# Kernel optimization log

Hardware: AMD Instinct MI355X
Metric: run time of the kernel (lower is better)

The kernel has to match this reference:

```python
import jax, jax.numpy as jnp
import numpy as np

B, S, D, H = 2, 2048, 1024, 16
HD = D // H  # head_size = 64


def setup_inputs() -> dict:
    key = jax.random.key(0)
    ks = jax.random.split(key, 11)
    s = 1.0 / np.sqrt(D)
    inp = {
        "q": jax.random.normal(ks[0], (B, S, D), jnp.float32),
        "k": jax.random.normal(ks[1], (B, S, D), jnp.float32),
        "v": jax.random.normal(ks[2], (B, S, D), jnp.float32),
        "Wq": jax.random.normal(ks[3], (D, D), jnp.float32) * s,
        "bq": jax.random.normal(ks[4], (D,), jnp.float32) * s,
        "Wk": jax.random.normal(ks[5], (D, D), jnp.float32) * s,
        "bk": jax.random.normal(ks[6], (D,), jnp.float32) * s,
        "Wv": jax.random.normal(ks[7], (D, D), jnp.float32) * s,
        "bv": jax.random.normal(ks[8], (D,), jnp.float32) * s,
        "Wo": jax.random.normal(ks[9], (D, D), jnp.float32) * s,
        "bo": jax.random.normal(ks[10], (D,), jnp.float32) * s,
    }
    return inp


def reference(q, k, v, Wq, bq, Wk, bk, Wv, bv, Wo, bo):
    # project and split heads: [B,S,D] -> [B,H,S,HD]
    def split_heads(x, W, b):
        y = x @ W.T + b
        return y.reshape(B, S, H, HD).transpose(0, 2, 1, 3)

    qh = split_heads(q, Wq, bq)
    kh = split_heads(k, Wk, bk)
    vh = split_heads(v, Wv, bv)

    scale = 1.0 / jnp.sqrt(jnp.asarray(HD, qh.dtype))
    scores = jnp.einsum("bhqd,bhkd->bhqk", qh, kh) * scale  # [B,H,S,S]
    weights = jax.nn.softmax(scores, axis=-1)
    out = jnp.einsum("bhqk,bhkd->bhqd", weights, vh)  # [B,H,S,HD]
    out = out.transpose(0, 2, 1, 3).reshape(B, S, D)
    return out @ Wo.T + bo
```

## Files before the change

### kernel.cpp

```cpp
#include <hip/hip_runtime.h>

typedef __attribute__((ext_vector_type(4))) float f32x4;
typedef __attribute__((ext_vector_type(8))) short bf16x8;
typedef __attribute__((ext_vector_type(8))) unsigned short u16x8;
typedef __attribute__((ext_vector_type(4))) unsigned short u16x4;
typedef __attribute__((ext_vector_type(4))) unsigned int u32x4;
typedef unsigned short ushort_t;

#define LOG2E 1.4426950408889634f

__device__ inline unsigned short f2bf(float x) {
  union { float f; unsigned int u; } v; v.f = x;
  unsigned int r = v.u + 0x7fffu + ((v.u >> 16) & 1u);
  return (unsigned short)(r >> 16);
}

__device__ inline unsigned cvtpk_bf16(float a, float b) {
  unsigned r;
  asm("v_cvt_pk_bf16_f32 %0, %1, %2" : "=v"(r) : "v"(a), "v"(b));
  return r;
}

__device__ inline void gload_lds16(const void* g, void* l) {
  __builtin_amdgcn_global_load_lds(
      (const __attribute__((address_space(1))) unsigned int*)g,
      (__attribute__((address_space(3))) unsigned int*)l, 16, 0, 0);
}

__device__ inline void cvt_body(const float* __restrict__ src, ushort_t* __restrict__ dst, int i) {
  const f32x4* s = (const f32x4*)src;
  f32x4 a = s[2 * i], b = s[2 * i + 1];
  u16x8 o;
#pragma unroll
  for (int j = 0; j < 4; ++j) { o[j] = f2bf(a[j]); o[4 + j] = f2bf(b[j]); }
  *(u16x8*)(dst + (size_t)i * 8) = o;
}

__global__ __launch_bounds__(256) void cvt_bf16(const float* __restrict__ src,
                                                ushort_t* __restrict__ dst, int n8) {
  int i = blockIdx.x * 256 + threadIdx.x;
  if (i < n8) cvt_body(src, dst, i);
}

__global__ __launch_bounds__(256) void cvt_all(const float* __restrict__ q,
                                               const float* __restrict__ k,
                                               const float* __restrict__ v,
                                               const float* __restrict__ Wq,
                                               const float* __restrict__ Wk,
                                               const float* __restrict__ Wv,
                                               const float* __restrict__ Wo,
                                               ushort_t* __restrict__ Xb,
                                               ushort_t* __restrict__ Wb, int nx8) {
  int i = blockIdx.x * 256 + threadIdx.x;
  int z = blockIdx.y;
  if (z < 3) {
    if (i < nx8) cvt_body(z == 0 ? q : (z == 1 ? k : v), Xb + (size_t)z * nx8 * 8, i);
  } else {
    int w = i >> 17, off = i & 131071;
    const float* s = w == 0 ? Wq : (w == 1 ? Wk : (w == 2 ? Wv : Wo));
    cvt_body(s, Wb + (size_t)w * 1048576, off);
  }
}

template <typename F>
__device__ inline void gemm_core64(const ushort_t* __restrict__ A, const ushort_t* __restrict__ W,
                                   int m0, int n0, ushort_t* As, ushort_t* Bs, F&& mfma_step) {
  constexpr int K = 1024;
  const int tid = threadIdx.x, lane = tid & 63, wid = tid >> 6;
  const int r8 = lane >> 3;
  const int p8 = lane & 7;
  const int scol = (p8 ^ r8) * 8;
  for (int k0 = 0; k0 < K; k0 += 64) {
#pragma unroll
    for (int c = 0; c < 4; ++c) {
      int i = wid * 4 + c;
      int row = i * 8 + r8;
      gload_lds16(A + (size_t)(m0 + row) * K + k0 + scol, &As[i * 512]);
      gload_lds16(W + (size_t)(n0 + row) * K + k0 + scol, &Bs[i * 512]);
    }
    __syncthreads();
    mfma_step(As, Bs);
    __syncthreads();
  }
}

__global__ __launch_bounds__(256) void proj_gemm(const ushort_t* __restrict__ Abase, int aStride,
                                                 const ushort_t* __restrict__ Wall, int wStride,
                                                 const float* __restrict__ bq,
                                                 const float* __restrict__ bk,
                                                 const float* __restrict__ bv, float qs,
                                                 ushort_t* __restrict__ outQ,
                                                 ushort_t* __restrict__ outK,
                                                 ushort_t* __restrict__ outV, int zofs) {
  __shared__ __attribute__((aligned(16))) ushort_t As[128 * 64];
  __shared__ __attribute__((aligned(16))) ushort_t Bs[128 * 64];
  const int z = blockIdx.z + zofs;
  const ushort_t* A = Abase + (size_t)z * aStride;
  const ushort_t* W = Wall + (size_t)z * wStride;
  const float* bias = z == 0 ? bq : (z == 1 ? bk : bv);
  const float scale = z == 0 ? qs : 1.0f;
  ushort_t* out = z == 0 ? outQ : (z == 1 ? outK : outV);
  const int mode = z == 2 ? 1 : 0;

  const int tid = threadIdx.x, lane = tid & 63, wid = tid >> 6;
  const int m0 = blockIdx.x * 128, n0 = blockIdx.y * 128;
  const int wm = wid >> 1, wn = wid & 1;
  const int qr = lane & 15, kq = lane >> 4;
  f32x4 acc[4][4] = {};

  gemm_core64(A, W, m0, n0, As, Bs, [&](ushort_t* as, ushort_t* bs) {
#pragma unroll
    for (int h = 0; h < 2; ++h) {
      bf16x8 a[4], b[4];
#pragma unroll
      for (int f = 0; f < 4; ++f) {
        int ra = wm * 64 + f * 16 + qr;
        a[f] = *(const bf16x8*)&as[ra * 64 + (((h * 4 + kq) ^ (ra & 7)) * 8)];
        int rb = wn * 64 + f * 16 + qr;
        b[f] = *(const bf16x8*)&bs[rb * 64 + (((h * 4 + kq) ^ (rb & 7)) * 8)];
      }
#pragma unroll
      for (int i = 0; i < 4; ++i)
#pragma unroll
        for (int j = 0; j < 4; ++j)
          acc[i][j] = __builtin_amdgcn_mfma_f32_16x16x32_bf16(a[i], b[j], acc[i][j], 0, 0, 0);
    }
  });

  const int cm = m0 + wm * 64, cn = n0 + wn * 64;
#pragma unroll
  for (int fn = 0; fn < 4; ++fn) {
    int n = cn + fn * 16 + qr;
    float bvv = bias[n];
    int h = n >> 6, hd = n & 63;
#pragma unroll
    for (int fm = 0; fm < 4; ++fm) {
      int m = cm + fm * 16 + kq * 4;
      if (mode == 0) {
#pragma unroll
        for (int r = 0; r < 4; ++r) {
          int mm = m + r, b = mm >> 11, s = mm & 2047;
          out[((size_t)(b * 16 + h) * 2048 + s) * 64 + hd] = f2bf((acc[fm][fn][r] + bvv) * scale);
        }
      } else {
        int b = m >> 11, s = m & 2047;
        u16x4 pk;
#pragma unroll
        for (int r = 0; r < 4; ++r) pk[r] = f2bf((acc[fm][fn][r] + bvv) * scale);
        *(u16x4*)&out[((size_t)(b * 16 + h) * 64 + hd) * 2048 + s] = pk;
      }
    }
  }
}

__global__ __launch_bounds__(256) void gemm_out(const ushort_t* __restrict__ A,
                                                const ushort_t* __restrict__ W,
                                                const float* __restrict__ bias,
                                                float* __restrict__ out) {
  __shared__ __attribute__((aligned(16))) ushort_t As[128 * 64];
  __shared__ __attribute__((aligned(16))) ushort_t Bs[128 * 64];
  const int tid = threadIdx.x, lane = tid & 63, wid = tid >> 6;
  const int m0 = blockIdx.x * 128, n0 = blockIdx.y * 128;
  const int wm = wid >> 1, wn = wid & 1;
  const int qr = lane & 15, kq = lane >> 4;
  f32x4 acc[4][4] = {};

  gemm_core64(A, W, m0, n0, As, Bs, [&](ushort_t* as, ushort_t* bs) {
#pragma unroll
    for (int h = 0; h < 2; ++h) {
      bf16x8 a[4], b[4];
#pragma unroll
      for (int f = 0; f < 4; ++f) {
        int ra = wm * 64 + f * 16 + qr;
        a[f] = *(const bf16x8*)&as[ra * 64 + (((h * 4 + kq) ^ (ra & 7)) * 8)];
        int rb = wn * 64 + f * 16 + qr;
        b[f] = *(const bf16x8*)&bs[rb * 64 + (((h * 4 + kq) ^ (rb & 7)) * 8)];
      }
#pragma unroll
      for (int i = 0; i < 4; ++i)
#pragma unroll
        for (int j = 0; j < 4; ++j)
          acc[i][j] = __builtin_amdgcn_mfma_f32_16x16x32_bf16(a[i], b[j], acc[i][j], 0, 0, 0);
    }
  });

  const int cm = m0 + wm * 64, cn = n0 + wn * 64;
#pragma unroll
  for (int fn = 0; fn < 4; ++fn) {
    int n = cn + fn * 16 + qr;
    float bvv = bias[n];
#pragma unroll
    for (int fm = 0; fm < 4; ++fm) {
      int m = cm + fm * 16 + kq * 4;
#pragma unroll
      for (int r = 0; r < 4; ++r) out[(size_t)(m + r) * 1024 + n] = acc[fm][fn][r] + bvv;
    }
  }
}

__global__ __launch_bounds__(256) void attn_fwd(const ushort_t* __restrict__ Qh,
                                                const ushort_t* __restrict__ Kh,
                                                const ushort_t* __restrict__ Vt,
                                                ushort_t* __restrict__ ctx) {
  constexpr int S = 2048, HD = 64, NT = S / 64;
  __shared__ __attribute__((aligned(16))) ushort_t Ks[2][64 * 64];
  __shared__ __attribute__((aligned(16))) ushort_t Vs[2][64 * 64];

  const int tid = threadIdx.x, lane = tid & 63, wid = tid >> 6;
  const int bh = blockIdx.y, qt = blockIdx.x;
  const size_t head = (size_t)bh * S * HD;
  const ushort_t* Qp = Qh + head;
  const ushort_t* Kp = Kh + head;
  const ushort_t* Vp = Vt + head;

  const int qr = lane & 15, kq = lane >> 4;
  const int q0 = qt * 64 + wid * 16;

  bf16x8 qf[2];
  qf[0] = *(const bf16x8*)&Qp[(size_t)(q0 + qr) * HD + kq * 8];
  qf[1] = *(const bf16x8*)&Qp[(size_t)(q0 + qr) * HD + 32 + kq * 8];

  f32x4 accO[4] = {};
  float mrun = -3e38f, lrun = 0.f;

  const int srow8 = lane >> 3, sp8 = lane & 7;

  for (int t = 0; t < NT; ++t) {
    const int buf = t & 1;
    {
      int kv0 = t == 0 ? 0 : (t + 1) * 64;
      int dbuf = t == 0 ? 0 : buf ^ 1;
      if (t == 0 || t + 1 < NT) {
#pragma unroll
        for (int c = 0; c < 2; ++c) {
          int i = wid * 2 + c;
          int row = i * 8 + srow8;
          int s = sp8 ^ (row & 7);
          gload_lds16(&Kp[(size_t)(kv0 + row) * HD + s * 8], &Ks[dbuf][i * 512]);
          gload_lds16(&Vp[(size_t)row * S + kv0 + s * 8], &Vs[dbuf][i * 512]);
        }
      }
      if (t == 0) {
        __syncthreads();
        if (NT > 1) {
#pragma unroll
          for (int c = 0; c < 2; ++c) {
            int i = wid * 2 + c;
            int row = i * 8 + srow8;
            int s = sp8 ^ (row & 7);
            gload_lds16(&Kp[(size_t)(64 + row) * HD + s * 8], &Ks[1][i * 512]);
            gload_lds16(&Vp[(size_t)row * S + 64 + s * 8], &Vs[1][i * 512]);
          }
        }
      }
    }

    f32x4 sc[4] = {};
    __builtin_amdgcn_s_setprio(1);
#pragma unroll
    for (int fn = 0; fn < 4; ++fn) {
      int rk = fn * 16 + qr;
#pragma unroll
      for (int kh = 0; kh < 2; ++kh) {
        bf16x8 kf = *(const bf16x8*)&Ks[buf][rk * 64 + (((kh * 4 + kq) ^ (rk & 7)) * 8)];
        sc[fn] = __builtin_amdgcn_mfma_f32_16x16x32_bf16(kf, qf[kh], sc[fn], 0, 0, 0);
      }
    }
    __builtin_amdgcn_s_setprio(0);

    float t0 = fmaxf(fmaxf(fmaxf(sc[0][0], sc[0][1]), sc[0][2]), sc[0][3]);
    float t1 = fmaxf(fmaxf(fmaxf(sc[1][0], sc[1][1]), sc[1][2]), sc[1][3]);
    float t2 = fmaxf(fmaxf(fmaxf(sc[2][0], sc[2][1]), sc[2][2]), sc[2][3]);
    float t3 = fmaxf(fmaxf(fmaxf(sc[3][0], sc[3][1]), sc[3][2]), sc[3][3]);
    float pm = fmaxf(fmaxf(t0, t1), fmaxf(t2, t3));
    pm = fmaxf(pm, __shfl_xor(pm, 16, 64));
    pm = fmaxf(pm, __shfl_xor(pm, 32, 64));

    bool need = pm > mrun + 8.0f;
    if (__any(need)) {
      float mn = need ? pm : mrun;
      float sf = __builtin_amdgcn_exp2f(mrun - mn);
      mrun = mn;
#pragma unroll
      for (int f2 = 0; f2 < 4; ++f2) accO[f2] *= sf;
      lrun *= sf;
    }

    float pv[4][4];
    float sum = 0.f;
#pragma unroll
    for (int fn = 0; fn < 4; ++fn)
#pragma unroll
      for (int r = 0; r < 4; ++r) {
        float p = __builtin_amdgcn_exp2f(sc[fn][r] - mrun);
        pv[fn][r] = p;
        sum += p;
      }
    sum += __shfl_xor(sum, 16, 64);
    sum += __shfl_xor(sum, 32, 64);
    lrun += sum;

    unsigned wv[4][2];
#pragma unroll
    for (int fn = 0; fn < 4; ++fn) {
      wv[fn][0] = cvtpk_bf16(pv[fn][0], pv[fn][1]);
      wv[fn][1] = cvtpk_bf16(pv[fn][2], pv[fn][3]);
    }

    __builtin_amdgcn_s_setprio(1);
#pragma unroll
    for (int ks = 0; ks < 2; ++ks) {
      unsigned a0 = wv[2 * ks][0], b0 = wv[2 * ks + 1][0];
      unsigned a1 = wv[2 * ks][1], b1 = wv[2 * ks + 1][1];
      asm volatile("v_permlane32_swap_b32 %0, %1" : "+v"(a0), "+v"(b0));
      asm volatile("v_permlane16_swap_b32 %0, %1" : "+v"(a0), "+v"(b0));
      asm volatile("v_permlane32_swap_b32 %0, %1" : "+v"(a1), "+v"(b1));
      asm volatile("v_permlane16_swap_b32 %0, %1" : "+v"(a1), "+v"(b1));
      u32x4 praw;
      praw[0] = a0; praw[1] = a1; praw[2] = b0; praw[3] = b1;
      bf16x8 pf = __builtin_bit_cast(bf16x8, praw);
#pragma unroll
      for (int f2 = 0; f2 < 4; ++f2) {
        int rv = f2 * 16 + qr;
        bf16x8 vf = *(const bf16x8*)&Vs[buf][rv * 64 + (((ks * 4 + kq) ^ (rv & 7)) * 8)];
        accO[f2] = __builtin_amdgcn_mfma_f32_16x16x32_bf16(vf, pf, accO[f2], 0, 0, 0);
      }
    }
    __builtin_amdgcn_s_setprio(0);
    __syncthreads();
  }

  float inv = 1.0f / lrun;
  const int b = bh >> 4, h = bh & 15;
#pragma unroll
  for (int f2 = 0; f2 < 4; ++f2) {
    u16x4 pk;
#pragma unroll
    for (int r = 0; r < 4; ++r) pk[r] = f2bf(accO[f2][r] * inv);
    int col = h * 64 + f2 * 16 + kq * 4;
    *(u16x4*)&ctx[((size_t)b * 2048 + q0 + qr) * 1024 + col] = pk;
  }
}

extern "C" void kernel_launch(void* const* d_in, const int* in_sizes, int n_in,
                              void* d_out, int out_size, void* d_ws, size_t ws_size,
                              hipStream_t stream) {
  const float* q = (const float*)d_in[0];
  const float* k = (const float*)d_in[1];
  const float* v = (const float*)d_in[2];
  const float* Wq = (const float*)d_in[3];
  const float* bq = (const float*)d_in[4];
  const float* Wk = (const float*)d_in[5];
  const float* bk = (const float*)d_in[6];
  const float* Wv = (const float*)d_in[7];
  const float* bv = (const float*)d_in[8];
  const float* Wo = (const float*)d_in[9];
  const float* bo = (const float*)d_in[10];

  char* ws = (char*)d_ws;
  const size_t MB = 1024 * 1024;
  const int NXE = 4194304;
  const int NWE = 1048576;
  const float qs = 0.125f * LOG2E;
  dim3 gg(32, 8), ga(32, 32);

  if (ws_size >= 56 * MB) {
    ushort_t* Xb = (ushort_t*)(ws);
    ushort_t* Wb = (ushort_t*)(ws + 24 * MB);
    ushort_t* Qh = (ushort_t*)(ws + 32 * MB);
    ushort_t* Kh = (ushort_t*)(ws + 40 * MB);
    ushort_t* Vt = (ushort_t*)(ws + 48 * MB);
    cvt_all<<<dim3(2048, 4), 256, 0, stream>>>(q, k, v, Wq, Wk, Wv, Wo, Xb, Wb, NXE / 8);
    proj_gemm<<<dim3(32, 8, 3), 256, 0, stream>>>(Xb, NXE, Wb, NWE, bq, bk, bv, qs,
                                                  Qh, Kh, Vt, 0);
    attn_fwd<<<ga, 256, 0, stream>>>(Qh, Kh, Vt, Xb);
    gemm_out<<<gg, 256, 0, stream>>>(Xb, Wb + (size_t)3 * NWE, bo, (float*)d_out);
  } else if (ws_size >= 40 * MB) {
    ushort_t* Xb = (ushort_t*)(ws);
    ushort_t* Wb = (ushort_t*)(ws + 8 * MB);
    ushort_t* Qh = (ushort_t*)(ws + 16 * MB);
    ushort_t* Kh = (ushort_t*)(ws + 24 * MB);
    ushort_t* Vt = (ushort_t*)(ws + 32 * MB);
    const float* xs[3] = {q, k, v};
    for (int z = 0; z < 3; ++z) {
      cvt_bf16<<<2048, 256, 0, stream>>>(xs[z], Xb, NXE / 8);
      if (z == 0)
        cvt_all<<<dim3(2048, 1), 256, 0, stream>>>(q, k, v, Wq, Wk, Wv, Wo, Xb, Wb, 0);
      proj_gemm<<<dim3(32, 8, 1), 256, 0, stream>>>(Xb, 0, Wb, NWE, bq, bk, bv, qs,
                                                    Qh, Kh, Vt, z);
    }
    attn_fwd<<<ga, 256, 0, stream>>>(Qh, Kh, Vt, Xb);
    gemm_out<<<gg, 256, 0, stream>>>(Xb, Wb + (size_t)3 * NWE, bo, (float*)d_out);
  } else {
    ushort_t* Xb = (ushort_t*)(ws);
    ushort_t* Wb = (ushort_t*)(ws + 8 * MB);
    ushort_t* Qh = (ushort_t*)(ws + 10 * MB);
    ushort_t* Kh = (ushort_t*)(ws + 18 * MB);
    ushort_t* Vt = (ushort_t*)(ws + 26 * MB);
    const float* xs[3] = {q, k, v};
    const float* wsrc[3] = {Wq, Wk, Wv};
    for (int z = 0; z < 3; ++z) {
      cvt_bf16<<<2048, 256, 0, stream>>>(xs[z], Xb, NXE / 8);
      cvt_bf16<<<512, 256, 0, stream>>>(wsrc[z], Wb, NWE / 8);
      proj_gemm<<<dim3(32, 8, 1), 256, 0, stream>>>(Xb, 0, Wb, 0, bq, bk, bv, qs,
                                                    Qh, Kh, Vt, z);
    }
    attn_fwd<<<ga, 256, 0, stream>>>(Qh, Kh, Vt, Xb);
    cvt_bf16<<<512, 256, 0, stream>>>(Wo, Wb, NWE / 8);
    gemm_out<<<gg, 256, 0, stream>>>(Xb, Wb, bo, (float*)d_out);
  }
}
```

Baseline: 150.5 us.

## Software-pipeline QK^T one tile ahead of softmax/PV in attention loop

Splits K and V staging and reorders the attention loop so the QK^T MFMAs for tile t+1 are issued before the softmax and PV of tile t, using two ping-pong score buffers. K and V loads for later tiles are staged separately and interleaved so each stays one or two tiles ahead. The goal is to overlap matrix-core work with softmax VALU work and hide LDS and global load latency. In exchange it holds more score registers live, which may raise register pressure and lower occupancy.

```diff
diff --git a/kernel.cpp b/kernel.cpp
--- a/kernel.cpp
+++ b/kernel.cpp
@@ -225,49 +225,40 @@
 
   const int srow8 = lane >> 3, sp8 = lane & 7;
 
-  for (int t = 0; t < NT; ++t) {
-    const int buf = t & 1;
-    {
-      int kv0 = t == 0 ? 0 : (t + 1) * 64;
-      int dbuf = t == 0 ? 0 : buf ^ 1;
-      if (t == 0 || t + 1 < NT) {
-#pragma unroll
-        for (int c = 0; c < 2; ++c) {
-          int i = wid * 2 + c;
-          int row = i * 8 + srow8;
-          int s = sp8 ^ (row & 7);
-          gload_lds16(&Kp[(size_t)(kv0 + row) * HD + s * 8], &Ks[dbuf][i * 512]);
-          gload_lds16(&Vp[(size_t)row * S + kv0 + s * 8], &Vs[dbuf][i * 512]);
-        }
-      }
-      if (t == 0) {
-        __syncthreads();
-        if (NT > 1) {
-#pragma unroll
-          for (int c = 0; c < 2; ++c) {
-            int i = wid * 2 + c;
-            int row = i * 8 + srow8;
-            int s = sp8 ^ (row & 7);
-            gload_lds16(&Kp[(size_t)(64 + row) * HD + s * 8], &Ks[1][i * 512]);
-            gload_lds16(&Vp[(size_t)row * S + 64 + s * 8], &Vs[1][i * 512]);
-          }
-        }
-      }
-    }
-
-    f32x4 sc[4] = {};
+  auto stageK = [&](int tt, int db) {
+#pragma unroll
+    for (int c = 0; c < 2; ++c) {
+      int i = wid * 2 + c;
+      int row = i * 8 + srow8;
+      int s = sp8 ^ (row & 7);
+      gload_lds16(&Kp[(size_t)(tt * 64 + row) * HD + s * 8], &Ks[db][i * 512]);
+    }
+  };
+  auto stageV = [&](int tt, int db) {
+#pragma unroll
+    for (int c = 0; c < 2; ++c) {
+      int i = wid * 2 + c;
+      int row = i * 8 + srow8;
+      int s = sp8 ^ (row & 7);
+      gload_lds16(&Vp[(size_t)row * S + tt * 64 + s * 8], &Vs[db][i * 512]);
+    }
+  };
+
+  auto qkt = [&](f32x4(&sc)[4], int kbuf) {
+    const f32x4 z = {};
     __builtin_amdgcn_s_setprio(1);
 #pragma unroll
     for (int fn = 0; fn < 4; ++fn) {
       int rk = fn * 16 + qr;
-#pragma unroll
-      for (int kh = 0; kh < 2; ++kh) {
-        bf16x8 kf = *(const bf16x8*)&Ks[buf][rk * 64 + (((kh * 4 + kq) ^ (rk & 7)) * 8)];
-        sc[fn] = __builtin_amdgcn_mfma_f32_16x16x32_bf16(kf, qf[kh], sc[fn], 0, 0, 0);
-      }
+      bf16x8 kf0 = *(const bf16x8*)&Ks[kbuf][rk * 64 + ((kq ^ (rk & 7)) * 8)];
+      sc[fn] = __builtin_amdgcn_mfma_f32_16x16x32_bf16(kf0, qf[0], z, 0, 0, 0);
+      bf16x8 kf1 = *(const bf16x8*)&Ks[kbuf][rk * 64 + (((4 + kq) ^ (rk & 7)) * 8)];
+      sc[fn] = __builtin_amdgcn_mfma_f32_16x16x32_bf16(kf1, qf[1], sc[fn], 0, 0, 0);
     }
     __builtin_amdgcn_s_setprio(0);
-
+  };
+
+  auto smaxpv = [&](f32x4(&sc)[4], int vbuf) {
     float t0 = fmaxf(fmaxf(fmaxf(sc[0][0], sc[0][1]), sc[0][2]), sc[0][3]);
     float t1 = fmaxf(fmaxf(fmaxf(sc[1][0], sc[1][1]), sc[1][2]), sc[1][3]);
     float t2 = fmaxf(fmaxf(fmaxf(sc[2][0], sc[2][1]), sc[2][2]), sc[2][3]);
@@ -322,11 +313,31 @@
 #pragma unroll
       for (int f2 = 0; f2 < 4; ++f2) {
         int rv = f2 * 16 + qr;
-        bf16x8 vf = *(const bf16x8*)&Vs[buf][rv * 64 + (((ks * 4 + kq) ^ (rv & 7)) * 8)];
+        bf16x8 vf = *(const bf16x8*)&Vs[vbuf][rv * 64 + (((ks * 4 + kq) ^ (rv & 7)) * 8)];
         accO[f2] = __builtin_amdgcn_mfma_f32_16x16x32_bf16(vf, pf, accO[f2], 0, 0, 0);
       }
     }
     __builtin_amdgcn_s_setprio(0);
+  };
+
+  stageK(0, 0);
+  stageV(0, 0);
+  __syncthreads();
+  stageK(1, 1);
+  f32x4 scA[4], scB[4];
+  qkt(scA, 0);
+  __syncthreads();
+
+  for (int t = 0; t < NT; t += 2) {
+    if (t + 1 < NT) stageV(t + 1, 1);
+    if (t + 2 < NT) stageK(t + 2, 0);
+    if (t + 1 < NT) qkt(scB, 1);
+    smaxpv(scA, 0);
+    __syncthreads();
+    if (t + 2 < NT) stageV(t + 2, 0);
+    if (t + 3 < NT) stageK(t + 3, 1);
+    if (t + 2 < NT) qkt(scA, 0);
+    smaxpv(scB, 1);
     __syncthreads();
   }
 
```

Result: no change. 151.7 us (+0.8%).

## Double-buffer projection GEMM LDS tiles with K=32 stages to overlap loads

Applied to the files above, without the earlier changes.

Replaces the single-buffer K=64 GEMM mainloop used by the QKV projection and output GEMMs with a double-buffered K=32 loop. The next tile's global-to-LDS loads are issued before the current tile's MFMAs, and only one barrier runs per step. This hides load latency behind compute, but halves the work per iteration and doubles the iteration count. The LDS swizzle is reworked for 32-wide rows.

```diff
diff --git a/kernel.cpp b/kernel.cpp
--- a/kernel.cpp
+++ b/kernel.cpp
@@ -63,23 +63,32 @@
 }
 
 template <typename F>
-__device__ inline void gemm_core64(const ushort_t* __restrict__ A, const ushort_t* __restrict__ W,
-                                   int m0, int n0, ushort_t* As, ushort_t* Bs, F&& mfma_step) {
+__device__ inline void gemm_core32(const ushort_t* __restrict__ A, const ushort_t* __restrict__ W,
+                                   int m0, int n0,
+                                   ushort_t (&As)[2][128 * 32], ushort_t (&Bs)[2][128 * 32],
+                                   F&& mfma_step) {
   constexpr int K = 1024;
   const int tid = threadIdx.x, lane = tid & 63, wid = tid >> 6;
-  const int r8 = lane >> 3;
-  const int p8 = lane & 7;
-  const int scol = (p8 ^ r8) * 8;
-  for (int k0 = 0; k0 < K; k0 += 64) {
-#pragma unroll
-    for (int c = 0; c < 4; ++c) {
-      int i = wid * 4 + c;
-      int row = i * 8 + r8;
-      gload_lds16(A + (size_t)(m0 + row) * K + k0 + scol, &As[i * 512]);
-      gload_lds16(W + (size_t)(n0 + row) * K + k0 + scol, &Bs[i * 512]);
-    }
-    __syncthreads();
-    mfma_step(As, Bs);
+  const int srow = lane >> 2;
+  const int sp = lane & 3;
+
+  auto stage = [&](int k0, int db) {
+#pragma unroll
+    for (int c = 0; c < 2; ++c) {
+      int i = wid * 2 + c;
+      int row = i * 16 + srow;
+      int s = sp ^ ((row >> 1) & 3);
+      gload_lds16(A + (size_t)(m0 + row) * K + k0 + s * 8, &As[db][i * 512]);
+      gload_lds16(W + (size_t)(n0 + row) * K + k0 + s * 8, &Bs[db][i * 512]);
+    }
+  };
+
+  stage(0, 0);
+  __syncthreads();
+  for (int k0 = 0; k0 < K; k0 += 32) {
+    const int buf = (k0 >> 5) & 1;
+    if (k0 + 32 < K) stage(k0 + 32, buf ^ 1);
+    mfma_step(As[buf], Bs[buf]);
     __syncthreads();
   }
 }
@@ -92,8 +101,8 @@
                                                  ushort_t* __restrict__ outQ,
                                                  ushort_t* __restrict__ outK,
                                                  ushort_t* __restrict__ outV, int zofs) {
-  __shared__ __attribute__((aligned(16))) ushort_t As[128 * 64];
-  __shared__ __attribute__((aligned(16))) ushort_t Bs[128 * 64];
+  __shared__ __attribute__((aligned(16))) ushort_t As[2][128 * 32];
+  __shared__ __attribute__((aligned(16))) ushort_t Bs[2][128 * 32];
   const int z = blockIdx.z + zofs;
   const ushort_t* A = Abase + (size_t)z * aStride;
   const ushort_t* W = Wall + (size_t)z * wStride;
@@ -108,23 +117,20 @@
   const int qr = lane & 15, kq = lane >> 4;
   f32x4 acc[4][4] = {};
 
-  gemm_core64(A, W, m0, n0, As, Bs, [&](ushort_t* as, ushort_t* bs) {
-#pragma unroll
-    for (int h = 0; h < 2; ++h) {
-      bf16x8 a[4], b[4];
-#pragma unroll
-      for (int f = 0; f < 4; ++f) {
-        int ra = wm * 64 + f * 16 + qr;
-        a[f] = *(const bf16x8*)&as[ra * 64 + (((h * 4 + kq) ^ (ra & 7)) * 8)];
-        int rb = wn * 64 + f * 16 + qr;
-        b[f] = *(const bf16x8*)&bs[rb * 64 + (((h * 4 + kq) ^ (rb & 7)) * 8)];
-      }
-#pragma unroll
-      for (int i = 0; i < 4; ++i)
-#pragma unroll
-        for (int j = 0; j < 4; ++j)
-          acc[i][j] = __builtin_amdgcn_mfma_f32_16x16x32_bf16(a[i], b[j], acc[i][j], 0, 0, 0);
-    }
+  gemm_core32(A, W, m0, n0, As, Bs, [&](ushort_t* as, ushort_t* bs) {
+    bf16x8 a[4], b[4];
+#pragma unroll
+    for (int f = 0; f < 4; ++f) {
+      int ra = wm * 64 + f * 16 + qr;
+      a[f] = *(const bf16x8*)&as[ra * 32 + (kq ^ ((ra >> 1) & 3)) * 8];
+      int rb = wn * 64 + f * 16 + qr;
+      b[f] = *(const bf16x8*)&bs[rb * 32 + (kq ^ ((rb >> 1) & 3)) * 8];
+    }
+#pragma unroll
+    for (int i = 0; i < 4; ++i)
+#pragma unroll
+      for (int j = 0; j < 4; ++j)
+        acc[i][j] = __builtin_amdgcn_mfma_f32_16x16x32_bf16(a[i], b[j], acc[i][j], 0, 0, 0);
   });
 
   const int cm = m0 + wm * 64, cn = n0 + wn * 64;
@@ -157,31 +163,28 @@
                                                 const ushort_t* __restrict__ W,
                                                 const float* __restrict__ bias,
                                                 float* __restrict__ out) {
-  __shared__ __attribute__((aligned(16))) ushort_t As[128 * 64];
-  __shared__ __attribute__((aligned(16))) ushort_t Bs[128 * 64];
+  __shared__ __attribute__((aligned(16))) ushort_t As[2][128 * 32];
+  __shared__ __attribute__((aligned(16))) ushort_t Bs[2][128 * 32];
   const int tid = threadIdx.x, lane = tid & 63, wid = tid >> 6;
   const int m0 = blockIdx.x * 128, n0 = blockIdx.y * 128;
   const int wm = wid >> 1, wn = wid & 1;
   const int qr = lane & 15, kq = lane >> 4;
   f32x4 acc[4][4] = {};
 
-  gemm_core64(A, W, m0, n0, As, Bs, [&](ushort_t* as, ushort_t* bs) {
-#pragma unroll
-    for (int h = 0; h < 2; ++h) {
-      bf16x8 a[4], b[4];
-#pragma unroll
-      for (int f = 0; f < 4; ++f) {
-        int ra = wm * 64 + f * 16 + qr;
-        a[f] = *(const bf16x8*)&as[ra * 64 + (((h * 4 + kq) ^ (ra & 7)) * 8)];
-        int rb = wn * 64 + f * 16 + qr;
-        b[f] = *(const bf16x8*)&bs[rb * 64 + (((h * 4 + kq) ^ (rb & 7)) * 8)];
-      }
-#pragma unroll
-      for (int i = 0; i < 4; ++i)
-#pragma unroll
-        for (int j = 0; j < 4; ++j)
-          acc[i][j] = __builtin_amdgcn_mfma_f32_16x16x32_bf16(a[i], b[j], acc[i][j], 0, 0, 0);
-    }
+  gemm_core32(A, W, m0, n0, As, Bs, [&](ushort_t* as, ushort_t* bs) {
+    bf16x8 a[4], b[4];
+#pragma unroll
+    for (int f = 0; f < 4; ++f) {
+      int ra = wm * 64 + f * 16 + qr;
+      a[f] = *(const bf16x8*)&as[ra * 32 + (kq ^ ((ra >> 1) & 3)) * 8];
+      int rb = wn * 64 + f * 16 + qr;
+      b[f] = *(const bf16x8*)&bs[rb * 32 + (kq ^ ((rb >> 1) & 3)) * 8];
+    }
+#pragma unroll
+    for (int i = 0; i < 4; ++i)
+#pragma unroll
+      for (int j = 0; j < 4; ++j)
+        acc[i][j] = __builtin_amdgcn_mfma_f32_16x16x32_bf16(a[i], b[j], acc[i][j], 0, 0, 0);
   });
 
   const int cm = m0 + wm * 64, cn = n0 + wn * 64;
```

Result: faster. 141.4 us (-6.0%).
